# Kernel optimization log

Measured on AMD Instinct MI355X. Metric: run time of the kernel, lower is better.

Reference implementation:

```python
import jax, jax.numpy as jnp
import numpy as np

B, S, D = 32, 512, 512
GH, LH = 8, 4            # global / local num_heads
W, STRIDE = 10, 5        # local window size and hop (window_size // 2)


def _mha(x, w_in, b_in, w_out, b_out, n_heads, key_mask=None):
    """Torch nn.MultiheadAttention (self-attn, eval mode). x: [N, L, D]."""
    N, L, d = x.shape
    dh = d // n_heads
    qkv = x @ w_in.T + b_in                       # [N, L, 3D]
    q, k, v = jnp.split(qkv, 3, axis=-1)
    def heads(t):
        return t.reshape(N, L, n_heads, dh).transpose(0, 2, 1, 3)  # [N,H,L,dh]
    q, k, v = heads(q), heads(k), heads(v)
    scores = jnp.einsum('bhqd,bhkd->bhqk', q, k) / jnp.sqrt(jnp.asarray(dh, x.dtype))
    if key_mask is not None:                      # key_mask: [N, L] bool, True = valid
        scores = jnp.where(key_mask[:, None, None, :], scores, jnp.asarray(-1e9, x.dtype))
    attn = jax.nn.softmax(scores, axis=-1)
    out = jnp.einsum('bhqk,bhkd->bhqd', attn, v).transpose(0, 2, 1, 3).reshape(N, L, d)
    return out @ w_out.T + b_out


def setup_inputs() -> dict:
    key = jax.random.key(0)
    ks = jax.random.split(key, 12)
    s = 0.02
    return {
        'x':      jax.random.normal(ks[0], (B, S, D), jnp.float32),
        'gw_in':  jax.random.normal(ks[1], (3 * D, D), jnp.float32) * s,
        'gb_in':  jnp.zeros((3 * D,), jnp.float32),
        'gw_out': jax.random.normal(ks[2], (D, D), jnp.float32) * s,
        'gb_out': jnp.zeros((D,), jnp.float32),
        'lw_in':  jax.random.normal(ks[3], (3 * D, D), jnp.float32) * s,
        'lb_in':  jnp.zeros((3 * D,), jnp.float32),
        'lw_out': jax.random.normal(ks[4], (D, D), jnp.float32) * s,
        'lb_out': jnp.zeros((D,), jnp.float32),
        'fw':     jax.random.normal(ks[5], (D, 2 * D), jnp.float32) * s,
        'fb':     jnp.zeros((D,), jnp.float32),
    }


def reference(x, gw_in, gb_in, gw_out, gb_out, lw_in, lb_in, lw_out, lb_out, fw, fb):
    # ---- global branch: full self-attention over the sequence ----
    global_out = _mha(x, gw_in, gb_in, gw_out, gb_out, GH)

    # ---- local branch: overlapping windows of size W, hop STRIDE ----
    starts = np.arange(0, S, STRIDE)              # static window starts
    NW = len(starts)
    pos = starts[:, None] + np.arange(W)          # [NW, W] absolute positions
    valid = pos < S                               # ragged tail windows
    idx = np.minimum(pos, S - 1)                  # clipped gather indices

    windows = x[:, idx]                           # [B, NW, W, D]
    windows = windows.reshape(B * NW, W, D)
    key_mask = jnp.broadcast_to(jnp.asarray(valid)[None], (B, NW, W)).reshape(B * NW, W)

    local_attn = _mha(windows, lw_in, lb_in, lw_out, lb_out, LH, key_mask=key_mask)
    local_attn = local_attn.reshape(B, NW, W, D) * jnp.asarray(valid)[None, :, :, None].astype(x.dtype)

    # scatter-add overlapping window outputs back (matches `local_out[:, i:end] +=`)
    local_out = jnp.zeros_like(x).at[:, idx.reshape(-1)].add(local_attn.reshape(B, NW * W, D))

    # ---- fusion MLP (dropout = identity in eval) ----
    combined = jnp.concatenate([global_out, local_out], axis=-1)   # [B, S, 2D]
    return jax.nn.relu(combined @ fw.T + fb)
```

## Files before the change

### kernel.cpp

```cpp
#include <hip/hip_runtime.h>
#include <cstdint>
#include <cstddef>

#define DEV __device__ __forceinline__

typedef float f32x4 __attribute__((ext_vector_type(4)));
typedef short bf16x8 __attribute__((ext_vector_type(8)));

DEV unsigned short f2bf(float f) {
  union { float f; unsigned u; } v; v.f = f;
  unsigned u = v.u;
  unsigned r = u + 0x7FFFu + ((u >> 16) & 1u);
  return (unsigned short)(r >> 16);
}
DEV float bf2f(unsigned short h) {
  union { unsigned u; float f; } v; v.u = ((unsigned)h) << 16;
  return v.f;
}
DEV unsigned cvtpk(float lo, float hi) {
  unsigned r;
  asm("v_cvt_pk_bf16_f32 %0, %1, %2" : "=v"(r) : "v"(lo), "v"(hi));
  return r;
}

DEV void gload16(const void* g, void* l) {
  __builtin_amdgcn_global_load_lds((const __attribute__((address_space(1))) unsigned int*)g,
                                   (__attribute__((address_space(3))) unsigned int*)l,
                                   16, 0, 0);
}

DEV f32x4 MFMA(bf16x8 a, bf16x8 b, f32x4 c) {
  return __builtin_amdgcn_mfma_f32_16x16x32_bf16(a, b, c, 0, 0, 0);
}

__global__ void k_f2bf(const float* __restrict__ src, unsigned short* __restrict__ dst, int n) {
  int i = (blockIdx.x * blockDim.x + threadIdx.x) * 4;
  int stride = gridDim.x * blockDim.x * 4;
  for (; i < n; i += stride) {
    float4 v = *(const float4*)(src + i);
    ushort4 o;
    o.x = f2bf(v.x); o.y = f2bf(v.y); o.z = f2bf(v.z); o.w = f2bf(v.w);
    *(ushort4*)(dst + i) = o;
  }
}

__global__ __launch_bounds__(256) void k_merge(const float* __restrict__ fw,
                                               const float* __restrict__ gw_out,
                                               const float* __restrict__ lw_out,
                                               unsigned short* __restrict__ M1b,
                                               unsigned short* __restrict__ M2b) {
  __shared__ float Fa[64][68];
  __shared__ float Gb[64][68];
  const int bi = blockIdx.x, bj = blockIdx.y, m2 = blockIdx.z;
  const float* g = m2 ? lw_out : gw_out;
  const int i0 = bi * 64, j0 = bj * 64;
  const int tid = threadIdx.x;
  const int tr = tid >> 4, tc = tid & 15;
  float acc[4][4] = {};
  for (int kc = 0; kc < 8; kc++) {
    int k0 = kc * 64;
    __syncthreads();
    #pragma unroll
    for (int it = 0; it < 4; it++) {
      int r = tr + 16 * it;
      float4 v = *(const float4*)(fw + (size_t)(i0 + r) * 1024 + m2 * 512 + k0 + tc * 4);
      Fa[tc * 4 + 0][r] = v.x; Fa[tc * 4 + 1][r] = v.y;
      Fa[tc * 4 + 2][r] = v.z; Fa[tc * 4 + 3][r] = v.w;
      *(float4*)&Gb[r][tc * 4] = *(const float4*)(g + (size_t)(k0 + r) * 512 + j0 + tc * 4);
    }
    __syncthreads();
    for (int k = 0; k < 64; k++) {
      float4 a4 = *(const float4*)&Fa[k][tr * 4];
      float4 b4 = *(const float4*)&Gb[k][tc * 4];
      float av[4] = {a4.x, a4.y, a4.z, a4.w};
      float bv[4] = {b4.x, b4.y, b4.z, b4.w};
      #pragma unroll
      for (int r = 0; r < 4; r++)
        #pragma unroll
        for (int c = 0; c < 4; c++)
          acc[r][c] += av[r] * bv[c];
    }
  }
  unsigned short* M = m2 ? M2b : M1b;
  #pragma unroll
  for (int r = 0; r < 4; r++) {
    ushort4 pk;
    pk.x = f2bf(acc[r][0]); pk.y = f2bf(acc[r][1]);
    pk.z = f2bf(acc[r][2]); pk.w = f2bf(acc[r][3]);
    *(ushort4*)&M[(size_t)(i0 + tr * 4 + r) * 512 + j0 + tc * 4] = pk;
  }
}

__global__ __launch_bounds__(256) void k_bias(const float* __restrict__ fw, const float* __restrict__ gb_out,
                                              const float* __restrict__ lb_out, const float* __restrict__ fb,
                                              float* __restrict__ bias1, float* __restrict__ bias2) {
  __shared__ float bv[512];
  const int which = blockIdx.y;
  const int i0 = blockIdx.x * 64;
  const float* src = which ? lb_out : gb_out;
  for (int t = threadIdx.x; t < 512; t += 256) bv[t] = src[t];
  __syncthreads();
  const int r = threadIdx.x >> 2, c4 = threadIdx.x & 3;
  const float* frow = fw + (size_t)(i0 + r) * 1024 + (which ? 512 : 0) + c4 * 128;
  float a = 0.f;
  #pragma unroll 4
  for (int k = 0; k < 128; k += 4) {
    float4 v = *(const float4*)(frow + k);
    a += v.x * bv[c4 * 128 + k] + v.y * bv[c4 * 128 + k + 1]
       + v.z * bv[c4 * 128 + k + 2] + v.w * bv[c4 * 128 + k + 3];
  }
  a += __shfl_xor(a, 1);
  a += __shfl_xor(a, 2);
  if (c4 == 0) {
    int i = i0 + r;
    if (which) bias2[i] = a;
    else       bias1[i] = a + fb[i];
  }
}

__global__ __launch_bounds__(256) void k_qkv(const unsigned short* __restrict__ A,
                                             const unsigned short* __restrict__ Wg,
                                             const unsigned short* __restrict__ Wl,
                                             const float* __restrict__ bias_g,
                                             const float* __restrict__ bias_l,
                                             float qs_g, float qs_l,
                                             unsigned short* __restrict__ Cg,
                                             unsigned short* __restrict__ Cl) {
  __shared__ unsigned short As[2][128 * 32];
  __shared__ unsigned short Bs[2][128 * 32];
  const int tid = threadIdx.x;
  const int wave = tid >> 6, lane = tid & 63;
  const int wr = wave >> 1, wc = wave & 1;
  const int bm = blockIdx.x;
  const bool isl = (blockIdx.y >= 12);
  const int bn = isl ? (int)blockIdx.y - 12 : (int)blockIdx.y;
  const unsigned short* Wm = isl ? Wl : Wg;
  const float* bias = isl ? bias_l : bias_g;
  const float qscale = isl ? qs_l : qs_g;
  unsigned short* C = isl ? Cl : Cg;
  const int ql = lane & 15, kg = lane >> 4;

  const int c0 = wave * 2;
  const int srow = lane >> 2;
  const int schunk = (lane & 3) ^ ((lane >> 3) & 3);

  auto stage = [&](int buf, int t) {
    int k0 = t * 32;
    #pragma unroll
    for (int i = 0; i < 2; i++) {
      int c = c0 + i;
      int row = c * 16 + srow;
      gload16(A + (size_t)(bm * 128 + row) * 512 + k0 + schunk * 8, &As[buf][c * 512 + lane * 8]);
      gload16(Wm + (size_t)(bn * 128 + row) * 512 + k0 + schunk * 8, &Bs[buf][c * 512 + lane * 8]);
    }
  };

  const int soff = (kg ^ ((ql >> 1) & 3)) * 8;

  f32x4 acc[4][4] = {};
  stage(0, 0);
  __syncthreads();
  for (int t = 0; t < 16; t++) {
    int buf = t & 1;
    if (t + 1 < 16) stage(buf ^ 1, t + 1);
    const unsigned short* as = As[buf];
    const unsigned short* bs = Bs[buf];
    bf16x8 af[4], bfr[4];
    #pragma unroll
    for (int m = 0; m < 4; m++)
      af[m] = *(const bf16x8*)&as[(wr * 64 + m * 16 + ql) * 32 + soff];
    #pragma unroll
    for (int n = 0; n < 4; n++)
      bfr[n] = *(const bf16x8*)&bs[(wc * 64 + n * 16 + ql) * 32 + soff];
    #pragma unroll
    for (int m = 0; m < 4; m++)
      #pragma unroll
      for (int n = 0; n < 4; n++)
        acc[m][n] = MFMA(af[m], bfr[n], acc[m][n]);
    __syncthreads();
  }

  const int row0 = bm * 128 + wr * 64;
  const int col0 = bn * 128 + wc * 64;
  #pragma unroll
  for (int m = 0; m < 4; m++)
    #pragma unroll
    for (int n = 0; n < 4; n++) {
      int col = col0 + n * 16 + ql;
      float bcol = bias[col];
      float qs = (col < 512) ? qscale : 1.0f;
      #pragma unroll
      for (int r = 0; r < 4; r++) {
        int row = row0 + m * 16 + kg * 4 + r;
        C[(size_t)row * 1536 + col] = f2bf((acc[m][n][r] + bcol) * qs);
      }
    }
}

__global__ __launch_bounds__(256) void k_fin(const unsigned short* __restrict__ A,
                                             const unsigned short* __restrict__ A2,
                                             const unsigned short* __restrict__ Wm,
                                             const unsigned short* __restrict__ W2,
                                             const float* __restrict__ bias,
                                             const float* __restrict__ bias2,
                                             float* __restrict__ Cout) {
  __shared__ unsigned short As[2][128 * 32];
  __shared__ unsigned short Bs[2][128 * 32];
  const int tid = threadIdx.x;
  const int wave = tid >> 6, lane = tid & 63;
  const int wr = wave >> 1, wc = wave & 1;
  const int bm = blockIdx.x, bn = blockIdx.y;
  const int ql = lane & 15, kg = lane >> 4;

  const int c0 = wave * 2;
  const int srow = lane >> 2;
  const int schunk = (lane & 3) ^ ((lane >> 3) & 3);

  auto stage = [&](int buf, int t) {
    const unsigned short* sA = A;
    const unsigned short* sW = Wm;
    int k0 = t * 32;
    if (t >= 16) { sA = A2; sW = W2; k0 = (t - 16) * 32; }
    #pragma unroll
    for (int i = 0; i < 2; i++) {
      int c = c0 + i;
      int row = c * 16 + srow;
      gload16(sA + (size_t)(bm * 128 + row) * 512 + k0 + schunk * 8, &As[buf][c * 512 + lane * 8]);
      gload16(sW + (size_t)(bn * 128 + row) * 512 + k0 + schunk * 8, &Bs[buf][c * 512 + lane * 8]);
    }
  };

  const int soff = (kg ^ ((ql >> 1) & 3)) * 8;

  f32x4 acc[4][4] = {};
  stage(0, 0);
  __syncthreads();
  for (int t = 0; t < 32; t++) {
    int buf = t & 1;
    if (t + 1 < 32) stage(buf ^ 1, t + 1);
    const unsigned short* as = As[buf];
    const unsigned short* bs = Bs[buf];
    bf16x8 af[4], bfr[4];
    #pragma unroll
    for (int m = 0; m < 4; m++)
      af[m] = *(const bf16x8*)&as[(wr * 64 + m * 16 + ql) * 32 + soff];
    #pragma unroll
    for (int n = 0; n < 4; n++)
      bfr[n] = *(const bf16x8*)&bs[(wc * 64 + n * 16 + ql) * 32 + soff];
    #pragma unroll
    for (int m = 0; m < 4; m++)
      #pragma unroll
      for (int n = 0; n < 4; n++)
        acc[m][n] = MFMA(af[m], bfr[n], acc[m][n]);
    __syncthreads();
  }

  const int row0 = bm * 128 + wr * 64;
  const int col0 = bn * 128 + wc * 64;
  #pragma unroll
  for (int m = 0; m < 4; m++)
    #pragma unroll
    for (int n = 0; n < 4; n++) {
      int col = col0 + n * 16 + ql;
      float b1 = bias[col], b2 = bias2[col];
      #pragma unroll
      for (int r = 0; r < 4; r++) {
        int row = row0 + m * 16 + kg * 4 + r;
        float cc = ((row & 511) < 5) ? 1.0f : 2.0f;
        float v = acc[m][n][r] + b1 + cc * b2;
        Cout[(size_t)row * 512 + col] = fmaxf(v, 0.0f);
      }
    }
}

__global__ __launch_bounds__(1024, 4) void k_attn_g(const unsigned short* __restrict__ QKV,
                                                    unsigned short* __restrict__ Og) {
  __shared__ unsigned short Klds[512 * 64];
  __shared__ unsigned short Vt[64 * 512];
  const int tid = threadIdx.x, wave = tid >> 6, lane = tid & 63;
  const int ql = lane & 15, kg = lane >> 4;
  const int h = blockIdx.x, b = blockIdx.y;
  const size_t tb = (size_t)b * 512;
  const size_t hoff = (size_t)h * 64;

  #pragma unroll
  for (int i = 0; i < 4; i++) {
    int instr = wave * 4 + i;
    int row = instr * 8 + (lane >> 3);
    int slot = lane & 7;
    int c = slot ^ (row & 7);
    gload16(QKV + (tb + row) * 1536 + 512 + hoff + c * 8, &Klds[instr * 512 + lane * 8]);
  }
  {
    int key = tid & 511;
    int cb = (tid >> 9) * 4;
    int k64 = key & 63;
    int f = k64 >> 4, kgv = (k64 >> 2) & 3, r = k64 & 3;
    int col = (key & ~63) + 32 * (f >> 1) + 4 * (f & 1) + 8 * kgv + r;
    const unsigned short* Vp = QKV + (tb + key) * 1536 + 1024 + hoff;
    #pragma unroll
    for (int c8 = 0; c8 < 4; c8++) {
      bf16x8 v8 = *(const bf16x8*)(Vp + (cb + c8) * 8);
      #pragma unroll
      for (int j = 0; j < 8; j++) {
        int d = (cb + c8) * 8 + j;
        Vt[d * 512 + (((col >> 3) ^ (d & 7)) * 8) + (col & 7)] = (unsigned short)v8[j];
      }
    }
  }
  bf16x8 qf[2][2];
  #pragma unroll
  for (int m = 0; m < 2; m++) {
    const unsigned short* Qp = QKV + (tb + wave * 32 + m * 16 + ql) * 1536 + hoff;
    qf[m][0] = *(const bf16x8*)(Qp + kg * 8);
    qf[m][1] = *(const bf16x8*)(Qp + 32 + kg * 8);
  }
  __syncthreads();

  float l_part[2] = {};
  f32x4 ot[2][4] = {};

  for (int kv = 0; kv < 8; kv++) {
    const int k0 = kv * 64;
    bf16x8 kf[4][2], vb[4][2];
    #pragma unroll
    for (int f = 0; f < 4; f++) {
      int row = k0 + 16 * f + ql;
      #pragma unroll
      for (int c = 0; c < 2; c++)
        kf[f][c] = *(const bf16x8*)&Klds[row * 64 + (((c * 4 + kg) ^ (row & 7)) * 8)];
      int d = 16 * f + ql;
      #pragma unroll
      for (int st = 0; st < 2; st++) {
        int cb_r = (k0 >> 3) + st * 4 + kg;
        vb[f][st] = *(const bf16x8*)&Vt[d * 512 + ((cb_r ^ (d & 7)) * 8)];
      }
    }
    #pragma unroll
    for (int m = 0; m < 2; m++) {
      f32x4 s[4] = {};
      #pragma unroll
      for (int f = 0; f < 4; f++) {
        s[f] = MFMA(kf[f][0], qf[m][0], s[f]);
        s[f] = MFMA(kf[f][1], qf[m][1], s[f]);
      }
      #pragma unroll
      for (int f = 0; f < 4; f++) {
        #pragma unroll
        for (int r = 0; r < 4; r++)
          s[f][r] = exp2f(s[f][r]);
        l_part[m] += (s[f][0] + s[f][1]) + (s[f][2] + s[f][3]);
      }
      #pragma unroll
      for (int st = 0; st < 2; st++) {
        union { unsigned w[4]; bf16x8 v; } pb;
        #pragma unroll
        for (int w = 0; w < 4; w++) {
          int f = 2 * st + (w >> 1);
          pb.w[w] = cvtpk(s[f][2 * (w & 1)], s[f][2 * (w & 1) + 1]);
        }
        #pragma unroll
        for (int fp = 0; fp < 4; fp++)
          ot[m][fp] = MFMA(vb[fp][st], pb.v, ot[m][fp]);
      }
    }
  }

  #pragma unroll
  for (int m = 0; m < 2; m++) {
    float l = l_part[m];
    l += __shfl_xor(l, 16);
    l += __shfl_xor(l, 32);
    float inv = 1.0f / l;
    size_t row = tb + wave * 32 + m * 16 + ql;
    #pragma unroll
    for (int fp = 0; fp < 4; fp++) {
      ushort4 st4;
      st4.x = f2bf(ot[m][fp][0] * inv);
      st4.y = f2bf(ot[m][fp][1] * inv);
      st4.z = f2bf(ot[m][fp][2] * inv);
      st4.w = f2bf(ot[m][fp][3] * inv);
      *(ushort4*)&Og[row * 512 + hoff + 16 * fp + 4 * kg] = st4;
    }
  }
}

__global__ __launch_bounds__(256) void k_attn_l(const unsigned short* __restrict__ QKV,
                                                unsigned short* __restrict__ Lacc) {
  __shared__ unsigned short Qs[5][520];
  __shared__ unsigned short Ks[15][520];
  __shared__ unsigned short Vs[15][520];
  __shared__ float Pb[2][4][5][13];
  const int w = blockIdx.x, b = blockIdx.y;
  const int p0 = 5 * w;
  const int tid = threadIdx.x;
  const size_t tbase = (size_t)b * 512;

  for (int c = tid; c < 35 * 64; c += 256) {
    int row = c >> 6, ch = (c & 63) * 8;
    if (row < 5) {
      int tok = min(p0 + row, 511);
      *(bf16x8*)&Qs[row][ch] = *(const bf16x8*)(QKV + (tbase + tok) * 1536 + ch);
    } else if (row < 20) {
      int rr = row - 5;
      int tok = min(max(p0 - 5 + rr, 0), 511);
      *(bf16x8*)&Ks[rr][ch] = *(const bf16x8*)(QKV + (tbase + tok) * 1536 + 512 + ch);
    } else {
      int rr = row - 20;
      int tok = min(max(p0 - 5 + rr, 0), 511);
      *(bf16x8*)&Vs[rr][ch] = *(const bf16x8*)(QKV + (tbase + tok) * 1536 + 1024 + ch);
    }
  }
  __syncthreads();

  #pragma unroll
  for (int rep = 0; rep < 2; rep++) {
    int idx = tid + rep * 256;
    if (idx < 400) {
      int j = idx % 10;
      int t1 = idx / 10;
      int q = t1 % 5;
      int t2 = t1 / 5;
      int h = t2 & 3;
      int win = t2 >> 2;
      int krow = win ? j : j + 5;
      int ktok = p0 - 5 + krow;
      float scv = -1e30f;
      bool ok = (win == 0 || w > 0) && (p0 + q < 512) && (ktok < 512);
      if (ok) {
        float acc = 0.f;
        const unsigned short* qp = &Qs[q][h * 128];
        const unsigned short* kp = &Ks[krow][h * 128];
        #pragma unroll
        for (int ck = 0; ck < 16; ck++) {
          bf16x8 q8 = *(const bf16x8*)(qp + ck * 8);
          bf16x8 k8 = *(const bf16x8*)(kp + ck * 8);
          #pragma unroll
          for (int e = 0; e < 8; e++)
            acc += bf2f((unsigned short)q8[e]) * bf2f((unsigned short)k8[e]);
        }
        scv = acc;
      }
      Pb[win][h][q][j] = scv;
    }
  }
  __syncthreads();

  if (tid < 40) {
    int q = tid % 5;
    int t2 = tid / 5;
    int h = t2 & 3;
    int win = t2 >> 2;
    float* row = &Pb[win][h][q][0];
    float mx = -1e30f;
    #pragma unroll
    for (int j = 0; j < 10; j++) mx = fmaxf(mx, row[j]);
    float e[10]; float su = 0.f;
    #pragma unroll
    for (int j = 0; j < 10; j++) {
      float v = row[j];
      float ej = (v <= -1e29f) ? 0.f : exp2f(v - mx);
      e[j] = ej; su += ej;
    }
    float inv = (su > 0.f) ? 1.0f / su : 0.f;
    #pragma unroll
    for (int j = 0; j < 10; j++) row[j] = e[j] * inv;
  }
  __syncthreads();

  {
    const int h = tid >> 6;
    const int d = tid * 2;
    for (int qq = 0; qq < 5; qq++) {
      int p = p0 + qq;
      if (p >= 512) break;
      float a0 = 0.f, a1 = 0.f;
      const float* P0 = &Pb[0][h][qq][0];
      #pragma unroll
      for (int j = 0; j < 10; j++) {
        float pw = P0[j];
        a0 += pw * bf2f(Vs[j + 5][d]);
        a1 += pw * bf2f(Vs[j + 5][d + 1]);
      }
      if (w > 0) {
        const float* P1 = &Pb[1][h][qq][0];
        #pragma unroll
        for (int j = 0; j < 10; j++) {
          float pw = P1[j];
          a0 += pw * bf2f(Vs[j][d]);
          a1 += pw * bf2f(Vs[j][d + 1]);
        }
      }
      ushort2 st; st.x = f2bf(a0); st.y = f2bf(a1);
      *(ushort2*)&Lacc[(tbase + p) * 512 + d] = st;
    }
  }
}

extern "C" void kernel_launch(void* const* d_in, const int* in_sizes, int n_in,
                              void* d_out, int out_size, void* d_ws, size_t ws_size,
                              hipStream_t stream) {
  const float* x      = (const float*)d_in[0];
  const float* gw_in  = (const float*)d_in[1];
  const float* gb_in  = (const float*)d_in[2];
  const float* gw_out = (const float*)d_in[3];
  const float* gb_out = (const float*)d_in[4];
  const float* lw_in  = (const float*)d_in[5];
  const float* lb_in  = (const float*)d_in[6];
  const float* lw_out = (const float*)d_in[7];
  const float* lb_out = (const float*)d_in[8];
  const float* fw     = (const float*)d_in[9];
  const float* fb     = (const float*)d_in[10];

  char* ws = (char*)d_ws;
  auto alloc = [&](size_t bytes) -> char* {
    char* p = ws;
    ws += (bytes + 255) & ~(size_t)255;
    return p;
  };
  unsigned short* xb     = (unsigned short*)alloc((size_t)16384 * 512 * 2);
  unsigned short* gwin_b = (unsigned short*)alloc((size_t)1536 * 512 * 2);
  unsigned short* lwin_b = (unsigned short*)alloc((size_t)1536 * 512 * 2);
  unsigned short* M1b    = (unsigned short*)alloc((size_t)512 * 512 * 2);
  unsigned short* M2b    = (unsigned short*)alloc((size_t)512 * 512 * 2);
  float* bias1           = (float*)alloc(512 * 4);
  float* bias2           = (float*)alloc(512 * 4);
  unsigned short* QKVg   = (unsigned short*)alloc((size_t)16384 * 1536 * 2);
  unsigned short* QKVl   = (unsigned short*)alloc((size_t)16384 * 1536 * 2);
  unsigned short* Og     = (unsigned short*)alloc((size_t)16384 * 512 * 2);
  unsigned short* La     = (unsigned short*)alloc((size_t)16384 * 512 * 2);

  k_f2bf<<<2048, 256, 0, stream>>>(x, xb, 16384 * 512);
  k_f2bf<<<128, 256, 0, stream>>>(gw_in, gwin_b, 1536 * 512);
  k_f2bf<<<128, 256, 0, stream>>>(lw_in, lwin_b, 1536 * 512);
  k_merge<<<dim3(8, 8, 2), 256, 0, stream>>>(fw, gw_out, lw_out, M1b, M2b);
  k_bias<<<dim3(8, 2), 256, 0, stream>>>(fw, gb_out, lb_out, fb, bias1, bias2);

  k_qkv<<<dim3(128, 24), 256, 0, stream>>>(xb, gwin_b, lwin_b, gb_in, lb_in,
                                           0.125f * 1.44269504f,
                                           0.08838834764831845f * 1.44269504f,
                                           QKVg, QKVl);
  k_attn_g<<<dim3(8, 32), 1024, 0, stream>>>(QKVg, Og);
  k_attn_l<<<dim3(103, 32), 256, 0, stream>>>(QKVl, La);

  k_fin<<<dim3(128, 4), 256, 0, stream>>>(Og, La, M1b, M2b, bias1, bias2, (float*)d_out);
}
```

Before: 216.3 us.

## Fuse x fp32-to-bf16 conversion into QKV GEMM and merge weight conversions

Result: slower. 222.4 us (+2.8%).

```diff
diff --git a/kernel.cpp b/kernel.cpp
--- a/kernel.cpp
+++ b/kernel.cpp
@@ -33,10 +33,14 @@
   return __builtin_amdgcn_mfma_f32_16x16x32_bf16(a, b, c, 0, 0, 0);
 }
 
-__global__ void k_f2bf(const float* __restrict__ src, unsigned short* __restrict__ dst, int n) {
-  int i = (blockIdx.x * blockDim.x + threadIdx.x) * 4;
-  int stride = gridDim.x * blockDim.x * 4;
-  for (; i < n; i += stride) {
+__global__ void k_f2bfW(const float* __restrict__ g, const float* __restrict__ l,
+                        unsigned short* __restrict__ gd, unsigned short* __restrict__ ld) {
+  const int half = 128 * 256 * 4;
+  int bid = blockIdx.x;
+  const float* src = (bid < 128) ? g : l;
+  unsigned short* dst = (bid < 128) ? gd : ld;
+  int i = (((bid & 127) * blockDim.x) + threadIdx.x) * 4;
+  for (; i < 1536 * 512; i += half) {
     float4 v = *(const float4*)(src + i);
     ushort4 o;
     o.x = f2bf(v.x); o.y = f2bf(v.y); o.z = f2bf(v.z); o.w = f2bf(v.w);
@@ -118,7 +122,7 @@
   }
 }
 
-__global__ __launch_bounds__(256) void k_qkv(const unsigned short* __restrict__ A,
+__global__ __launch_bounds__(256) void k_qkv(const float* __restrict__ X,
                                              const unsigned short* __restrict__ Wg,
                                              const unsigned short* __restrict__ Wl,
                                              const float* __restrict__ bias_g,
@@ -144,13 +148,32 @@
   const int srow = lane >> 2;
   const int schunk = (lane & 3) ^ ((lane >> 3) & 3);
 
-  auto stage = [&](int buf, int t) {
+  const float* Xr0 = X + (size_t)(bm * 128 + c0 * 16 + srow) * 512 + schunk * 8;
+  const float* Xr1 = X + (size_t)(bm * 128 + (c0 + 1) * 16 + srow) * 512 + schunk * 8;
+
+  float4 a0a, a0b, a1a, a1b;
+  auto loadA = [&](int t) {
+    int k0 = t * 32;
+    a0a = *(const float4*)(Xr0 + k0);
+    a0b = *(const float4*)(Xr0 + k0 + 4);
+    a1a = *(const float4*)(Xr1 + k0);
+    a1b = *(const float4*)(Xr1 + k0 + 4);
+  };
+  auto writeA = [&](int buf) {
+    union { unsigned w[4]; bf16x8 v; } p0, p1;
+    p0.w[0] = cvtpk(a0a.x, a0a.y); p0.w[1] = cvtpk(a0a.z, a0a.w);
+    p0.w[2] = cvtpk(a0b.x, a0b.y); p0.w[3] = cvtpk(a0b.z, a0b.w);
+    p1.w[0] = cvtpk(a1a.x, a1a.y); p1.w[1] = cvtpk(a1a.z, a1a.w);
+    p1.w[2] = cvtpk(a1b.x, a1b.y); p1.w[3] = cvtpk(a1b.z, a1b.w);
+    *(bf16x8*)&As[buf][c0 * 512 + lane * 8] = p0.v;
+    *(bf16x8*)&As[buf][(c0 + 1) * 512 + lane * 8] = p1.v;
+  };
+  auto stageW = [&](int buf, int t) {
     int k0 = t * 32;
     #pragma unroll
     for (int i = 0; i < 2; i++) {
       int c = c0 + i;
       int row = c * 16 + srow;
-      gload16(A + (size_t)(bm * 128 + row) * 512 + k0 + schunk * 8, &As[buf][c * 512 + lane * 8]);
       gload16(Wm + (size_t)(bn * 128 + row) * 512 + k0 + schunk * 8, &Bs[buf][c * 512 + lane * 8]);
     }
   };
@@ -158,11 +181,13 @@
   const int soff = (kg ^ ((ql >> 1) & 3)) * 8;
 
   f32x4 acc[4][4] = {};
-  stage(0, 0);
+  loadA(0);
+  stageW(0, 0);
+  writeA(0);
   __syncthreads();
   for (int t = 0; t < 16; t++) {
     int buf = t & 1;
-    if (t + 1 < 16) stage(buf ^ 1, t + 1);
+    if (t + 1 < 16) { loadA(t + 1); stageW(buf ^ 1, t + 1); }
     const unsigned short* as = As[buf];
     const unsigned short* bs = Bs[buf];
     bf16x8 af[4], bfr[4];
@@ -177,6 +202,7 @@
       #pragma unroll
       for (int n = 0; n < 4; n++)
         acc[m][n] = MFMA(af[m], bfr[n], acc[m][n]);
+    if (t + 1 < 16) writeA(buf ^ 1);
     __syncthreads();
   }
 
@@ -518,7 +544,6 @@
     ws += (bytes + 255) & ~(size_t)255;
     return p;
   };
-  unsigned short* xb     = (unsigned short*)alloc((size_t)16384 * 512 * 2);
   unsigned short* gwin_b = (unsigned short*)alloc((size_t)1536 * 512 * 2);
   unsigned short* lwin_b = (unsigned short*)alloc((size_t)1536 * 512 * 2);
   unsigned short* M1b    = (unsigned short*)alloc((size_t)512 * 512 * 2);
@@ -530,13 +555,11 @@
   unsigned short* Og     = (unsigned short*)alloc((size_t)16384 * 512 * 2);
   unsigned short* La     = (unsigned short*)alloc((size_t)16384 * 512 * 2);
 
-  k_f2bf<<<2048, 256, 0, stream>>>(x, xb, 16384 * 512);
-  k_f2bf<<<128, 256, 0, stream>>>(gw_in, gwin_b, 1536 * 512);
-  k_f2bf<<<128, 256, 0, stream>>>(lw_in, lwin_b, 1536 * 512);
+  k_f2bfW<<<256, 256, 0, stream>>>(gw_in, lw_in, gwin_b, lwin_b);
   k_merge<<<dim3(8, 8, 2), 256, 0, stream>>>(fw, gw_out, lw_out, M1b, M2b);
   k_bias<<<dim3(8, 2), 256, 0, stream>>>(fw, gb_out, lb_out, fb, bias1, bias2);
 
-  k_qkv<<<dim3(128, 24), 256, 0, stream>>>(xb, gwin_b, lwin_b, gb_in, lb_in,
+  k_qkv<<<dim3(128, 24), 256, 0, stream>>>(x, gwin_b, lwin_b, gb_in, lb_in,
                                            0.125f * 1.44269504f,
                                            0.08838834764831845f * 1.44269504f,
                                            QKVg, QKVl);
```

## Merge prep kernels and global/local attention kernels into fewer launches

Applied to the files above, without the earlier changes.

After: 221.8 us. 1.03x slower.

```diff
diff --git a/kernel.cpp b/kernel.cpp
--- a/kernel.cpp
+++ b/kernel.cpp
@@ -33,88 +33,109 @@
   return __builtin_amdgcn_mfma_f32_16x16x32_bf16(a, b, c, 0, 0, 0);
 }
 
-__global__ void k_f2bf(const float* __restrict__ src, unsigned short* __restrict__ dst, int n) {
-  int i = (blockIdx.x * blockDim.x + threadIdx.x) * 4;
-  int stride = gridDim.x * blockDim.x * 4;
-  for (; i < n; i += stride) {
-    float4 v = *(const float4*)(src + i);
-    ushort4 o;
-    o.x = f2bf(v.x); o.y = f2bf(v.y); o.z = f2bf(v.z); o.w = f2bf(v.w);
-    *(ushort4*)(dst + i) = o;
-  }
-}
-
-__global__ __launch_bounds__(256) void k_merge(const float* __restrict__ fw,
-                                               const float* __restrict__ gw_out,
-                                               const float* __restrict__ lw_out,
-                                               unsigned short* __restrict__ M1b,
-                                               unsigned short* __restrict__ M2b) {
+__global__ __launch_bounds__(256) void k_prep(const float* __restrict__ x,
+                                              const float* __restrict__ gw_in,
+                                              const float* __restrict__ lw_in,
+                                              const float* __restrict__ fw,
+                                              const float* __restrict__ gw_out,
+                                              const float* __restrict__ lw_out,
+                                              const float* __restrict__ gb_out,
+                                              const float* __restrict__ lb_out,
+                                              const float* __restrict__ fb,
+                                              unsigned short* __restrict__ xb,
+                                              unsigned short* __restrict__ gwin_b,
+                                              unsigned short* __restrict__ lwin_b,
+                                              unsigned short* __restrict__ M1b,
+                                              unsigned short* __restrict__ M2b,
+                                              float* __restrict__ bias1,
+                                              float* __restrict__ bias2) {
   __shared__ float Fa[64][68];
   __shared__ float Gb[64][68];
-  const int bi = blockIdx.x, bj = blockIdx.y, m2 = blockIdx.z;
-  const float* g = m2 ? lw_out : gw_out;
-  const int i0 = bi * 64, j0 = bj * 64;
-  const int tid = threadIdx.x;
-  const int tr = tid >> 4, tc = tid & 15;
-  float acc[4][4] = {};
-  for (int kc = 0; kc < 8; kc++) {
-    int k0 = kc * 64;
-    __syncthreads();
-    #pragma unroll
-    for (int it = 0; it < 4; it++) {
-      int r = tr + 16 * it;
-      float4 v = *(const float4*)(fw + (size_t)(i0 + r) * 1024 + m2 * 512 + k0 + tc * 4);
-      Fa[tc * 4 + 0][r] = v.x; Fa[tc * 4 + 1][r] = v.y;
-      Fa[tc * 4 + 2][r] = v.z; Fa[tc * 4 + 3][r] = v.w;
-      *(float4*)&Gb[r][tc * 4] = *(const float4*)(g + (size_t)(k0 + r) * 512 + j0 + tc * 4);
-    }
-    __syncthreads();
-    for (int k = 0; k < 64; k++) {
-      float4 a4 = *(const float4*)&Fa[k][tr * 4];
-      float4 b4 = *(const float4*)&Gb[k][tc * 4];
-      float av[4] = {a4.x, a4.y, a4.z, a4.w};
-      float bv[4] = {b4.x, b4.y, b4.z, b4.w};
-      #pragma unroll
-      for (int r = 0; r < 4; r++)
-        #pragma unroll
-        for (int c = 0; c < 4; c++)
-          acc[r][c] += av[r] * bv[c];
-    }
-  }
-  unsigned short* M = m2 ? M2b : M1b;
-  #pragma unroll
-  for (int r = 0; r < 4; r++) {
-    ushort4 pk;
-    pk.x = f2bf(acc[r][0]); pk.y = f2bf(acc[r][1]);
-    pk.z = f2bf(acc[r][2]); pk.w = f2bf(acc[r][3]);
-    *(ushort4*)&M[(size_t)(i0 + tr * 4 + r) * 512 + j0 + tc * 4] = pk;
-  }
-}
-
-__global__ __launch_bounds__(256) void k_bias(const float* __restrict__ fw, const float* __restrict__ gb_out,
-                                              const float* __restrict__ lb_out, const float* __restrict__ fb,
-                                              float* __restrict__ bias1, float* __restrict__ bias2) {
   __shared__ float bv[512];
-  const int which = blockIdx.y;
-  const int i0 = blockIdx.x * 64;
-  const float* src = which ? lb_out : gb_out;
-  for (int t = threadIdx.x; t < 512; t += 256) bv[t] = src[t];
-  __syncthreads();
-  const int r = threadIdx.x >> 2, c4 = threadIdx.x & 3;
-  const float* frow = fw + (size_t)(i0 + r) * 1024 + (which ? 512 : 0) + c4 * 128;
-  float a = 0.f;
-  #pragma unroll 4
-  for (int k = 0; k < 128; k += 4) {
-    float4 v = *(const float4*)(frow + k);
-    a += v.x * bv[c4 * 128 + k] + v.y * bv[c4 * 128 + k + 1]
-       + v.z * bv[c4 * 128 + k + 2] + v.w * bv[c4 * 128 + k + 3];
-  }
-  a += __shfl_xor(a, 1);
-  a += __shfl_xor(a, 2);
-  if (c4 == 0) {
-    int i = i0 + r;
-    if (which) bias2[i] = a;
-    else       bias1[i] = a + fb[i];
+  const int bid = blockIdx.x, tid = threadIdx.x;
+
+  if (bid < 2048) {
+    int i = (bid * 256 + tid) * 4;
+    const int stride = 2048 * 256 * 4;
+    for (; i < 16384 * 512; i += stride) {
+      float4 v = *(const float4*)(x + i);
+      ushort4 o;
+      o.x = f2bf(v.x); o.y = f2bf(v.y); o.z = f2bf(v.z); o.w = f2bf(v.w);
+      *(ushort4*)(xb + i) = o;
+    }
+  } else if (bid < 2304) {
+    int b2 = bid - 2048;
+    const float* src = (b2 < 128) ? gw_in : lw_in;
+    unsigned short* dst = (b2 < 128) ? gwin_b : lwin_b;
+    int i = (((b2 & 127) * 256) + tid) * 4;
+    for (; i < 1536 * 512; i += 128 * 256 * 4) {
+      float4 v = *(const float4*)(src + i);
+      ushort4 o;
+      o.x = f2bf(v.x); o.y = f2bf(v.y); o.z = f2bf(v.z); o.w = f2bf(v.w);
+      *(ushort4*)(dst + i) = o;
+    }
+  } else if (bid < 2432) {
+    const int idx = bid - 2304;
+    const int m2 = idx >> 6, bi = (idx >> 3) & 7, bj = idx & 7;
+    const float* g = m2 ? lw_out : gw_out;
+    const int i0 = bi * 64, j0 = bj * 64;
+    const int tr = tid >> 4, tc = tid & 15;
+    float acc[4][4] = {};
+    for (int kc = 0; kc < 8; kc++) {
+      int k0 = kc * 64;
+      __syncthreads();
+      #pragma unroll
+      for (int it = 0; it < 4; it++) {
+        int r = tr + 16 * it;
+        float4 v = *(const float4*)(fw + (size_t)(i0 + r) * 1024 + m2 * 512 + k0 + tc * 4);
+        Fa[tc * 4 + 0][r] = v.x; Fa[tc * 4 + 1][r] = v.y;
+        Fa[tc * 4 + 2][r] = v.z; Fa[tc * 4 + 3][r] = v.w;
+        *(float4*)&Gb[r][tc * 4] = *(const float4*)(g + (size_t)(k0 + r) * 512 + j0 + tc * 4);
+      }
+      __syncthreads();
+      for (int k = 0; k < 64; k++) {
+        float4 a4 = *(const float4*)&Fa[k][tr * 4];
+        float4 b4 = *(const float4*)&Gb[k][tc * 4];
+        float av[4] = {a4.x, a4.y, a4.z, a4.w};
+        float bw[4] = {b4.x, b4.y, b4.z, b4.w};
+        #pragma unroll
+        for (int r = 0; r < 4; r++)
+          #pragma unroll
+          for (int c = 0; c < 4; c++)
+            acc[r][c] += av[r] * bw[c];
+      }
+    }
+    unsigned short* M = m2 ? M2b : M1b;
+    #pragma unroll
+    for (int r = 0; r < 4; r++) {
+      ushort4 pk;
+      pk.x = f2bf(acc[r][0]); pk.y = f2bf(acc[r][1]);
+      pk.z = f2bf(acc[r][2]); pk.w = f2bf(acc[r][3]);
+      *(ushort4*)&M[(size_t)(i0 + tr * 4 + r) * 512 + j0 + tc * 4] = pk;
+    }
+  } else {
+    const int idx = bid - 2432;
+    const int which = idx >> 3;
+    const int i0 = (idx & 7) * 64;
+    const float* src = which ? lb_out : gb_out;
+    for (int t = tid; t < 512; t += 256) bv[t] = src[t];
+    __syncthreads();
+    const int r = tid >> 2, c4 = tid & 3;
+    const float* frow = fw + (size_t)(i0 + r) * 1024 + (which ? 512 : 0) + c4 * 128;
+    float a = 0.f;
+    #pragma unroll 4
+    for (int k = 0; k < 128; k += 4) {
+      float4 v = *(const float4*)(frow + k);
+      a += v.x * bv[c4 * 128 + k] + v.y * bv[c4 * 128 + k + 1]
+         + v.z * bv[c4 * 128 + k + 2] + v.w * bv[c4 * 128 + k + 3];
+    }
+    a += __shfl_xor(a, 1);
+    a += __shfl_xor(a, 2);
+    if (c4 == 0) {
+      int i = i0 + r;
+      if (which) bias2[i] = a;
+      else       bias1[i] = a + fb[i];
+    }
   }
 }
 
@@ -273,226 +294,238 @@
     }
 }
 
-__global__ __launch_bounds__(1024, 4) void k_attn_g(const unsigned short* __restrict__ QKV,
-                                                    unsigned short* __restrict__ Og) {
-  __shared__ unsigned short Klds[512 * 64];
-  __shared__ unsigned short Vt[64 * 512];
-  const int tid = threadIdx.x, wave = tid >> 6, lane = tid & 63;
-  const int ql = lane & 15, kg = lane >> 4;
-  const int h = blockIdx.x, b = blockIdx.y;
-  const size_t tb = (size_t)b * 512;
-  const size_t hoff = (size_t)h * 64;
-
-  #pragma unroll
-  for (int i = 0; i < 4; i++) {
-    int instr = wave * 4 + i;
-    int row = instr * 8 + (lane >> 3);
-    int slot = lane & 7;
-    int c = slot ^ (row & 7);
-    gload16(QKV + (tb + row) * 1536 + 512 + hoff + c * 8, &Klds[instr * 512 + lane * 8]);
-  }
-  {
-    int key = tid & 511;
-    int cb = (tid >> 9) * 4;
-    int k64 = key & 63;
-    int f = k64 >> 4, kgv = (k64 >> 2) & 3, r = k64 & 3;
-    int col = (key & ~63) + 32 * (f >> 1) + 4 * (f & 1) + 8 * kgv + r;
-    const unsigned short* Vp = QKV + (tb + key) * 1536 + 1024 + hoff;
-    #pragma unroll
-    for (int c8 = 0; c8 < 4; c8++) {
-      bf16x8 v8 = *(const bf16x8*)(Vp + (cb + c8) * 8);
-      #pragma unroll
-      for (int j = 0; j < 8; j++) {
-        int d = (cb + c8) * 8 + j;
-        Vt[d * 512 + (((col >> 3) ^ (d & 7)) * 8) + (col & 7)] = (unsigned short)v8[j];
-      }
-    }
-  }
-  bf16x8 qf[2][2];
-  #pragma unroll
-  for (int m = 0; m < 2; m++) {
-    const unsigned short* Qp = QKV + (tb + wave * 32 + m * 16 + ql) * 1536 + hoff;
-    qf[m][0] = *(const bf16x8*)(Qp + kg * 8);
-    qf[m][1] = *(const bf16x8*)(Qp + 32 + kg * 8);
-  }
-  __syncthreads();
-
-  float l_part[2] = {};
-  f32x4 ot[2][4] = {};
-
-  for (int kv = 0; kv < 8; kv++) {
-    const int k0 = kv * 64;
-    bf16x8 kf[4][2], vb[4][2];
-    #pragma unroll
-    for (int f = 0; f < 4; f++) {
-      int row = k0 + 16 * f + ql;
-      #pragma unroll
-      for (int c = 0; c < 2; c++)
-        kf[f][c] = *(const bf16x8*)&Klds[row * 64 + (((c * 4 + kg) ^ (row & 7)) * 8)];
-      int d = 16 * f + ql;
-      #pragma unroll
-      for (int st = 0; st < 2; st++) {
-        int cb_r = (k0 >> 3) + st * 4 + kg;
-        vb[f][st] = *(const bf16x8*)&Vt[d * 512 + ((cb_r ^ (d & 7)) * 8)];
-      }
-    }
+__global__ __launch_bounds__(1024, 4) void k_attn(const unsigned short* __restrict__ QKVg,
+                                                  const unsigned short* __restrict__ QKVl,
+                                                  unsigned short* __restrict__ Og,
+                                                  unsigned short* __restrict__ La) {
+  __shared__ __align__(16) unsigned char smem[153920];
+  const int tid = threadIdx.x;
+  const int bid = blockIdx.x;
+
+  if (bid < 256) {
+    unsigned short* Klds = (unsigned short*)smem;
+    unsigned short* Vt   = (unsigned short*)(smem + 65536);
+    const int wave = tid >> 6, lane = tid & 63;
+    const int ql = lane & 15, kg = lane >> 4;
+    const int h = bid & 7, b = bid >> 3;
+    const size_t tb = (size_t)b * 512;
+    const size_t hoff = (size_t)h * 64;
+
+    #pragma unroll
+    for (int i = 0; i < 4; i++) {
+      int instr = wave * 4 + i;
+      int row = instr * 8 + (lane >> 3);
+      int slot = lane & 7;
+      int c = slot ^ (row & 7);
+      gload16(QKVg + (tb + row) * 1536 + 512 + hoff + c * 8, &Klds[instr * 512 + lane * 8]);
+    }
+    {
+      int key = tid & 511;
+      int cb = (tid >> 9) * 4;
+      int k64 = key & 63;
+      int f = k64 >> 4, kgv = (k64 >> 2) & 3, r = k64 & 3;
+      int col = (key & ~63) + 32 * (f >> 1) + 4 * (f & 1) + 8 * kgv + r;
+      const unsigned short* Vp = QKVg + (tb + key) * 1536 + 1024 + hoff;
+      #pragma unroll
+      for (int c8 = 0; c8 < 4; c8++) {
+        bf16x8 v8 = *(const bf16x8*)(Vp + (cb + c8) * 8);
+        #pragma unroll
+        for (int j = 0; j < 8; j++) {
+          int d = (cb + c8) * 8 + j;
+          Vt[d * 512 + (((col >> 3) ^ (d & 7)) * 8) + (col & 7)] = (unsigned short)v8[j];
+        }
+      }
+    }
+    bf16x8 qf[2][2];
     #pragma unroll
     for (int m = 0; m < 2; m++) {
-      f32x4 s[4] = {};
+      const unsigned short* Qp = QKVg + (tb + wave * 32 + m * 16 + ql) * 1536 + hoff;
+      qf[m][0] = *(const bf16x8*)(Qp + kg * 8);
+      qf[m][1] = *(const bf16x8*)(Qp + 32 + kg * 8);
+    }
+    __syncthreads();
+
+    float l_part[2] = {};
+    f32x4 ot[2][4] = {};
+
+    for (int kv = 0; kv < 8; kv++) {
+      const int k0 = kv * 64;
+      bf16x8 kf[4][2], vb[4][2];
       #pragma unroll
       for (int f = 0; f < 4; f++) {
-        s[f] = MFMA(kf[f][0], qf[m][0], s[f]);
-        s[f] = MFMA(kf[f][1], qf[m][1], s[f]);
-      }
-      #pragma unroll
-      for (int f = 0; f < 4; f++) {
-        #pragma unroll
-        for (int r = 0; r < 4; r++)
-          s[f][r] = exp2f(s[f][r]);
-        l_part[m] += (s[f][0] + s[f][1]) + (s[f][2] + s[f][3]);
-      }
-      #pragma unroll
-      for (int st = 0; st < 2; st++) {
-        union { unsigned w[4]; bf16x8 v; } pb;
-        #pragma unroll
-        for (int w = 0; w < 4; w++) {
-          int f = 2 * st + (w >> 1);
-          pb.w[w] = cvtpk(s[f][2 * (w & 1)], s[f][2 * (w & 1) + 1]);
-        }
-        #pragma unroll
-        for (int fp = 0; fp < 4; fp++)
-          ot[m][fp] = MFMA(vb[fp][st], pb.v, ot[m][fp]);
-      }
-    }
-  }
-
-  #pragma unroll
-  for (int m = 0; m < 2; m++) {
-    float l = l_part[m];
-    l += __shfl_xor(l, 16);
-    l += __shfl_xor(l, 32);
-    float inv = 1.0f / l;
-    size_t row = tb + wave * 32 + m * 16 + ql;
-    #pragma unroll
-    for (int fp = 0; fp < 4; fp++) {
-      ushort4 st4;
-      st4.x = f2bf(ot[m][fp][0] * inv);
-      st4.y = f2bf(ot[m][fp][1] * inv);
-      st4.z = f2bf(ot[m][fp][2] * inv);
-      st4.w = f2bf(ot[m][fp][3] * inv);
-      *(ushort4*)&Og[row * 512 + hoff + 16 * fp + 4 * kg] = st4;
-    }
-  }
-}
-
-__global__ __launch_bounds__(256) void k_attn_l(const unsigned short* __restrict__ QKV,
-                                                unsigned short* __restrict__ Lacc) {
-  __shared__ unsigned short Qs[5][520];
-  __shared__ unsigned short Ks[15][520];
-  __shared__ unsigned short Vs[15][520];
-  __shared__ float Pb[2][4][5][13];
-  const int w = blockIdx.x, b = blockIdx.y;
-  const int p0 = 5 * w;
-  const int tid = threadIdx.x;
-  const size_t tbase = (size_t)b * 512;
-
-  for (int c = tid; c < 35 * 64; c += 256) {
-    int row = c >> 6, ch = (c & 63) * 8;
-    if (row < 5) {
-      int tok = min(p0 + row, 511);
-      *(bf16x8*)&Qs[row][ch] = *(const bf16x8*)(QKV + (tbase + tok) * 1536 + ch);
-    } else if (row < 20) {
-      int rr = row - 5;
-      int tok = min(max(p0 - 5 + rr, 0), 511);
-      *(bf16x8*)&Ks[rr][ch] = *(const bf16x8*)(QKV + (tbase + tok) * 1536 + 512 + ch);
-    } else {
-      int rr = row - 20;
-      int tok = min(max(p0 - 5 + rr, 0), 511);
-      *(bf16x8*)&Vs[rr][ch] = *(const bf16x8*)(QKV + (tbase + tok) * 1536 + 1024 + ch);
-    }
-  }
-  __syncthreads();
-
-  #pragma unroll
-  for (int rep = 0; rep < 2; rep++) {
-    int idx = tid + rep * 256;
-    if (idx < 400) {
-      int j = idx % 10;
-      int t1 = idx / 10;
-      int q = t1 % 5;
-      int t2 = t1 / 5;
+        int row = k0 + 16 * f + ql;
+        #pragma unroll
+        for (int c = 0; c < 2; c++)
+          kf[f][c] = *(const bf16x8*)&Klds[row * 64 + (((c * 4 + kg) ^ (row & 7)) * 8)];
+        int d = 16 * f + ql;
+        #pragma unroll
+        for (int st = 0; st < 2; st++) {
+          int cb_r = (k0 >> 3) + st * 4 + kg;
+          vb[f][st] = *(const bf16x8*)&Vt[d * 512 + ((cb_r ^ (d & 7)) * 8)];
+        }
+      }
+      #pragma unroll
+      for (int m = 0; m < 2; m++) {
+        f32x4 s[4] = {};
+        #pragma unroll
+        for (int f = 0; f < 4; f++) {
+          s[f] = MFMA(kf[f][0], qf[m][0], s[f]);
+          s[f] = MFMA(kf[f][1], qf[m][1], s[f]);
+        }
+        #pragma unroll
+        for (int f = 0; f < 4; f++) {
+          #pragma unroll
+          for (int r = 0; r < 4; r++)
+            s[f][r] = exp2f(s[f][r]);
+          l_part[m] += (s[f][0] + s[f][1]) + (s[f][2] + s[f][3]);
+        }
+        #pragma unroll
+        for (int st = 0; st < 2; st++) {
+          union { unsigned w[4]; bf16x8 v; } pb;
+          #pragma unroll
+          for (int w = 0; w < 4; w++) {
+            int f = 2 * st + (w >> 1);
+            pb.w[w] = cvtpk(s[f][2 * (w & 1)], s[f][2 * (w & 1) + 1]);
+          }
+          #pragma unroll
+          for (int fp = 0; fp < 4; fp++)
+            ot[m][fp] = MFMA(vb[fp][st], pb.v, ot[m][fp]);
+        }
+      }
+    }
+
+    #pragma unroll
+    for (int m = 0; m < 2; m++) {
+      float l = l_part[m];
+      l += __shfl_xor(l, 16);
+      l += __shfl_xor(l, 32);
+      float inv = 1.0f / l;
+      size_t row = tb + wave * 32 + m * 16 + ql;
+      #pragma unroll
+      for (int fp = 0; fp < 4; fp++) {
+        ushort4 st4;
+        st4.x = f2bf(ot[m][fp][0] * inv);
+        st4.y = f2bf(ot[m][fp][1] * inv);
+        st4.z = f2bf(ot[m][fp][2] * inv);
+        st4.w = f2bf(ot[m][fp][3] * inv);
+        *(ushort4*)&Og[row * 512 + hoff + 16 * fp + 4 * kg] = st4;
+      }
+    }
+  } else {
+    const int idx = bid - 256;
+    const int wg = idx % 26, b = idx / 26;
+    const int sub = tid >> 8, st = tid & 255;
+    const int w = wg * 4 + sub;
+    const int p0 = 5 * w;
+    const bool act = (w < 103);
+    unsigned short* Qs = (unsigned short*)(smem + sub * 38480);
+    unsigned short* Ks = Qs + 2600;
+    unsigned short* Vs = Qs + 10400;
+    float* Pb = (float*)((unsigned char*)Qs + 36400);
+    const size_t tbase = (size_t)b * 512;
+
+    if (act) {
+      for (int c = st; c < 35 * 64; c += 256) {
+        int row = c >> 6, ch = (c & 63) * 8;
+        if (row < 5) {
+          int tok = min(p0 + row, 511);
+          *(bf16x8*)&Qs[row * 520 + ch] = *(const bf16x8*)(QKVl + (tbase + tok) * 1536 + ch);
+        } else if (row < 20) {
+          int rr = row - 5;
+          int tok = min(max(p0 - 5 + rr, 0), 511);
+          *(bf16x8*)&Ks[rr * 520 + ch] = *(const bf16x8*)(QKVl + (tbase + tok) * 1536 + 512 + ch);
+        } else {
+          int rr = row - 20;
+          int tok = min(max(p0 - 5 + rr, 0), 511);
+          *(bf16x8*)&Vs[rr * 520 + ch] = *(const bf16x8*)(QKVl + (tbase + tok) * 1536 + 1024 + ch);
+        }
+      }
+    }
+    __syncthreads();
+
+    if (act) {
+      #pragma unroll
+      for (int rep = 0; rep < 2; rep++) {
+        int id2 = st + rep * 256;
+        if (id2 < 400) {
+          int j = id2 % 10;
+          int t1 = id2 / 10;
+          int q = t1 % 5;
+          int t2 = t1 / 5;
+          int h = t2 & 3;
+          int win = t2 >> 2;
+          int krow = win ? j : j + 5;
+          int ktok = p0 - 5 + krow;
+          float scv = -1e30f;
+          bool ok = (win == 0 || w > 0) && (p0 + q < 512) && (ktok < 512);
+          if (ok) {
+            float acc = 0.f;
+            const unsigned short* qp = &Qs[q * 520 + h * 128];
+            const unsigned short* kp = &Ks[krow * 520 + h * 128];
+            #pragma unroll
+            for (int ck = 0; ck < 16; ck++) {
+              bf16x8 q8 = *(const bf16x8*)(qp + ck * 8);
+              bf16x8 k8 = *(const bf16x8*)(kp + ck * 8);
+              #pragma unroll
+              for (int e = 0; e < 8; e++)
+                acc += bf2f((unsigned short)q8[e]) * bf2f((unsigned short)k8[e]);
+            }
+            scv = acc;
+          }
+          Pb[win * 260 + h * 65 + q * 13 + j] = scv;
+        }
+      }
+    }
+    __syncthreads();
+
+    if (act && st < 40) {
+      int q = st % 5;
+      int t2 = st / 5;
       int h = t2 & 3;
       int win = t2 >> 2;
-      int krow = win ? j : j + 5;
-      int ktok = p0 - 5 + krow;
-      float scv = -1e30f;
-      bool ok = (win == 0 || w > 0) && (p0 + q < 512) && (ktok < 512);
-      if (ok) {
-        float acc = 0.f;
-        const unsigned short* qp = &Qs[q][h * 128];
-        const unsigned short* kp = &Ks[krow][h * 128];
-        #pragma unroll
-        for (int ck = 0; ck < 16; ck++) {
-          bf16x8 q8 = *(const bf16x8*)(qp + ck * 8);
-          bf16x8 k8 = *(const bf16x8*)(kp + ck * 8);
+      float* row = &Pb[win * 260 + h * 65 + q * 13];
+      float mx = -1e30f;
+      #pragma unroll
+      for (int j = 0; j < 10; j++) mx = fmaxf(mx, row[j]);
+      float e[10]; float su = 0.f;
+      #pragma unroll
+      for (int j = 0; j < 10; j++) {
+        float v = row[j];
+        float ej = (v <= -1e29f) ? 0.f : exp2f(v - mx);
+        e[j] = ej; su += ej;
+      }
+      float inv = (su > 0.f) ? 1.0f / su : 0.f;
+      #pragma unroll
+      for (int j = 0; j < 10; j++) row[j] = e[j] * inv;
+    }
+    __syncthreads();
+
+    if (act) {
+      const int h = st >> 6;
+      const int d = st * 2;
+      for (int qq = 0; qq < 5; qq++) {
+        int p = p0 + qq;
+        if (p >= 512) break;
+        float a0 = 0.f, a1 = 0.f;
+        const float* P0 = &Pb[h * 65 + qq * 13];
+        #pragma unroll
+        for (int j = 0; j < 10; j++) {
+          float pw = P0[j];
+          a0 += pw * bf2f(Vs[(j + 5) * 520 + d]);
+          a1 += pw * bf2f(Vs[(j + 5) * 520 + d + 1]);
+        }
+        if (w > 0) {
+          const float* P1 = &Pb[260 + h * 65 + qq * 13];
           #pragma unroll
-          for (int e = 0; e < 8; e++)
-            acc += bf2f((unsigned short)q8[e]) * bf2f((unsigned short)k8[e]);
-        }
-        scv = acc;
-      }
-      Pb[win][h][q][j] = scv;
-    }
-  }
-  __syncthreads();
-
-  if (tid < 40) {
-    int q = tid % 5;
-    int t2 = tid / 5;
-    int h = t2 & 3;
-    int win = t2 >> 2;
-    float* row = &Pb[win][h][q][0];
-    float mx = -1e30f;
-    #pragma unroll
-    for (int j = 0; j < 10; j++) mx = fmaxf(mx, row[j]);
-    float e[10]; float su = 0.f;
-    #pragma unroll
-    for (int j = 0; j < 10; j++) {
-      float v = row[j];
-      float ej = (v <= -1e29f) ? 0.f : exp2f(v - mx);
-      e[j] = ej; su += ej;
-    }
-    float inv = (su > 0.f) ? 1.0f / su : 0.f;
-    #pragma unroll
-    for (int j = 0; j < 10; j++) row[j] = e[j] * inv;
-  }
-  __syncthreads();
-
-  {
-    const int h = tid >> 6;
-    const int d = tid * 2;
-    for (int qq = 0; qq < 5; qq++) {
-      int p = p0 + qq;
-      if (p >= 512) break;
-      float a0 = 0.f, a1 = 0.f;
-      const float* P0 = &Pb[0][h][qq][0];
-      #pragma unroll
-      for (int j = 0; j < 10; j++) {
-        float pw = P0[j];
-        a0 += pw * bf2f(Vs[j + 5][d]);
-        a1 += pw * bf2f(Vs[j + 5][d + 1]);
-      }
-      if (w > 0) {
-        const float* P1 = &Pb[1][h][qq][0];
-        #pragma unroll
-        for (int j = 0; j < 10; j++) {
-          float pw = P1[j];
-          a0 += pw * bf2f(Vs[j][d]);
-          a1 += pw * bf2f(Vs[j][d + 1]);
-        }
-      }
-      ushort2 st; st.x = f2bf(a0); st.y = f2bf(a1);
-      *(ushort2*)&Lacc[(tbase + p) * 512 + d] = st;
+          for (int j = 0; j < 10; j++) {
+            float pw = P1[j];
+            a0 += pw * bf2f(Vs[j * 520 + d]);
+            a1 += pw * bf2f(Vs[j * 520 + d + 1]);
+          }
+        }
+        ushort2 o2; o2.x = f2bf(a0); o2.y = f2bf(a1);
+        *(ushort2*)&La[(tbase + p) * 512 + d] = o2;
+      }
     }
   }
 }
@@ -530,18 +563,15 @@
   unsigned short* Og     = (unsigned short*)alloc((size_t)16384 * 512 * 2);
   unsigned short* La     = (unsigned short*)alloc((size_t)16384 * 512 * 2);
 
-  k_f2bf<<<2048, 256, 0, stream>>>(x, xb, 16384 * 512);
-  k_f2bf<<<128, 256, 0, stream>>>(gw_in, gwin_b, 1536 * 512);
-  k_f2bf<<<128, 256, 0, stream>>>(lw_in, lwin_b, 1536 * 512);
-  k_merge<<<dim3(8, 8, 2), 256, 0, stream>>>(fw, gw_out, lw_out, M1b, M2b);
-  k_bias<<<dim3(8, 2), 256, 0, stream>>>(fw, gb_out, lb_out, fb, bias1, bias2);
+  k_prep<<<2448, 256, 0, stream>>>(x, gw_in, lw_in, fw, gw_out, lw_out, gb_out, lb_out, fb,
+                                   xb, gwin_b, lwin_b, M1b, M2b, bias1, bias2);
 
   k_qkv<<<dim3(128, 24), 256, 0, stream>>>(xb, gwin_b, lwin_b, gb_in, lb_in,
                                            0.125f * 1.44269504f,
                                            0.08838834764831845f * 1.44269504f,
                                            QKVg, QKVl);
-  k_attn_g<<<dim3(8, 32), 1024, 0, stream>>>(QKVg, Og);
-  k_attn_l<<<dim3(103, 32), 256, 0, stream>>>(QKVl, La);
+
+  k_attn<<<1088, 1024, 0, stream>>>(QKVg, QKVl, Og, La);
 
   k_fin<<<dim3(128, 4), 256, 0, stream>>>(Og, La, M1b, M2b, bias1, bias2, (float*)d_out);
 }
```
